# Kernel tuning notes

Measured on AMD Instinct MI355X. Metric: run time of the kernel, lower is better.

The kernel has to match this reference:

```python
import jax, jax.numpy as jnp
import numpy as np
import math

B, LQ, C = 4, 2048, 256
NH, NL, NP = 8, 4, 8
HD = C // NH
SHAPES = [(128, 128), (64, 64), (32, 32), (16, 16)]


def _grid_init_bias():
    thetas = np.arange(NH, dtype=np.float32) * (2.0 * math.pi / NH)
    g = np.stack([np.cos(thetas), np.sin(thetas)], -1)
    g = g / np.abs(g).max(-1, keepdims=True)
    g = np.tile(g[:, None, None, :], (1, NL, NP, 1))
    g = g * ((np.arange(NP, dtype=np.float32) + 1.0) / NP)[None, None, :, None]
    return jnp.asarray(g.reshape(-1), jnp.float32)


def setup_inputs() -> dict:
    key = jax.random.key(0)
    ks = jax.random.split(key, 12)
    Lv = sum(h * w for h, w in SHAPES)
    query = jax.random.normal(ks[0], (B, LQ, C), jnp.float32)
    reference_points = jax.random.uniform(ks[1], (B, LQ, NL, 2), jnp.float32)
    value = jax.random.normal(ks[2], (B, Lv, C), jnp.float32)
    spatial_shapes = jnp.asarray(np.array(SHAPES, np.int32))
    starts = np.cumsum([0] + [h * w for h, w in SHAPES])[:-1]
    level_start_index = jnp.asarray(starts.astype(np.int32))
    OFF = NH * NL * NP * 2
    return {
        'query': query,
        'reference_points': reference_points,
        'value': value,
        'spatial_shapes': spatial_shapes,
        'level_start_index': level_start_index,
        'W_off': jax.random.normal(ks[3], (C, OFF), jnp.float32) * 0.01,
        'b_off': _grid_init_bias(),
        'W_attn': jax.random.normal(ks[4], (C, NH * NL * NP), jnp.float32) * 0.01,
        'b_attn': jnp.zeros((NH * NL * NP,), jnp.float32),
        'Wa1': jax.random.normal(ks[5], (C, C // 2), jnp.float32) * 0.02,
        'ba1': jnp.zeros((C // 2,), jnp.float32),
        'Wa2': jax.random.normal(ks[6], (C // 2, OFF), jnp.float32) * 0.02,
        'ba2': jnp.zeros((OFF,), jnp.float32),
        'Wv': jax.random.normal(ks[7], (C, C), jnp.float32) * (1.0 / math.sqrt(C)),
        'bv': jnp.zeros((C,), jnp.float32),
        'Wo': jax.random.normal(ks[8], (C, C), jnp.float32) * (1.0 / math.sqrt(C)),
        'bo': jnp.zeros((C,), jnp.float32),
    }


def _bilinear(vflat, gx, gy, H, W):
    # vflat: [B, nh, H*W, hd]; gx, gy: [B, Lq, nh, P] in grid coords [-1, 1]
    # Matches F.grid_sample(mode='bilinear', padding_mode='zeros', align_corners=False)
    Bq, Lq, nh, P = gx.shape
    hd = vflat.shape[-1]
    x = ((gx + 1.0) * W - 1.0) * 0.5
    y = ((gy + 1.0) * H - 1.0) * 0.5
    x0f = jnp.floor(x); y0f = jnp.floor(y)
    lx = x - x0f; ly = y - y0f
    x0 = x0f.astype(jnp.int32); y0 = y0f.astype(jnp.int32)
    out = jnp.zeros((Bq, Lq, nh, P, hd), vflat.dtype)
    corners = ((0, 0, (1 - lx) * (1 - ly)), (1, 0, lx * (1 - ly)),
               (0, 1, (1 - lx) * ly), (1, 1, lx * ly))
    for dx, dy, w in corners:
        xi = x0 + dx; yi = y0 + dy
        valid = (xi >= 0) & (xi < W) & (yi >= 0) & (yi < H)
        idx = jnp.clip(yi, 0, H - 1) * W + jnp.clip(xi, 0, W - 1)
        idx_t = idx.transpose(0, 2, 1, 3).reshape(Bq, nh, Lq * P)
        g = jnp.take_along_axis(vflat, idx_t[..., None], axis=2)  # [B, nh, Lq*P, hd]
        g = g.reshape(Bq, nh, Lq, P, hd).transpose(0, 2, 1, 3, 4)
        out = out + g * (w * valid.astype(vflat.dtype))[..., None]
    return out


def reference(query, reference_points, value, spatial_shapes, level_start_index,
              W_off, b_off, W_attn, b_attn, Wa1, ba1, Wa2, ba2, Wv, bv, Wo, bo):
    shapes = np.asarray(spatial_shapes)
    starts = np.asarray(level_start_index)
    Bq, Lq, _ = query.shape

    v = (value @ Wv + bv).reshape(Bq, -1, NH, HD)            # [B, Lv, nh, hd]
    off = (query @ W_off + b_off).reshape(Bq, Lq, NH, NL, NP, 2)
    hid = jax.nn.relu(query @ Wa1 + ba1)
    off = off + 0.1 * (hid @ Wa2 + ba2).reshape(Bq, Lq, NH, NL, NP, 2)
    aw = jax.nn.softmax((query @ W_attn + b_attn).reshape(Bq, Lq, NH, NL * NP), -1)
    aw = aw.reshape(Bq, Lq, NH, NL, NP)

    # offset normalizer is (W, H) per level
    norm = jnp.stack([spatial_shapes[:, 1], spatial_shapes[:, 0]], -1).astype(query.dtype)
    loc = reference_points[:, :, None, :, None, :] + off / norm[None, None, None, :, None, :]
    grid = loc * 2.0 - 1.0                                    # [B, Lq, nh, NL, NP, 2]

    acc = jnp.zeros((Bq, Lq, NH, HD), query.dtype)
    for lvl in range(NL):
        H, W = int(shapes[lvl, 0]), int(shapes[lvl, 1])
        s = int(starts[lvl]); e = s + H * W
        vl = v[:, s:e].transpose(0, 2, 1, 3)                  # [B, nh, H*W, hd]
        gx = grid[:, :, :, lvl, :, 0]
        gy = grid[:, :, :, lvl, :, 1]
        samp = _bilinear(vl, gx, gy, H, W)                    # [B, Lq, nh, P, hd]
        acc = acc + jnp.einsum('blhpd,blhp->blhd', samp, aw[:, :, :, lvl, :])
    out = acc.reshape(Bq, Lq, NH * HD)
    return out @ Wo + bo
```

## Files before the change

kernel.cpp:

```cpp
#include <hip/hip_runtime.h>
#include <math.h>

#define B_SZ 4
#define LQ_SZ 2048
#define C_SZ 256
#define NH_SZ 8
#define NL_SZ 4
#define NP_SZ 8
#define HD_SZ 32
#define LV_SZ 21760
#define NQ_SZ (B_SZ * LQ_SZ)
#define MV_SZ (B_SZ * LV_SZ)

typedef __attribute__((ext_vector_type(8))) short bf16x8;
typedef __attribute__((ext_vector_type(8))) unsigned short ushort8;
typedef __attribute__((ext_vector_type(4))) float f32x4;

__device__ __forceinline__ float bf2f(unsigned short u) {
  union { float f; unsigned v; } x;
  x.v = ((unsigned)u) << 16;
  return x.f;
}
__device__ __forceinline__ unsigned short f2bf(float f) {
  union { float f; unsigned v; } x;
  x.f = f;
  unsigned r = x.v + 0x7fffu + ((x.v >> 16) & 1u);
  return (unsigned short)(r >> 16);
}

__device__ __forceinline__ bf16x8 cvt8(f32x4 a, f32x4 b) {
  union { unsigned u[4]; bf16x8 v; } r;
  asm("v_cvt_pk_bf16_f32 %0, %1, %2" : "=v"(r.u[0]) : "v"(a[0]), "v"(a[1]));
  asm("v_cvt_pk_bf16_f32 %0, %1, %2" : "=v"(r.u[1]) : "v"(a[2]), "v"(a[3]));
  asm("v_cvt_pk_bf16_f32 %0, %1, %2" : "=v"(r.u[2]) : "v"(b[0]), "v"(b[1]));
  asm("v_cvt_pk_bf16_f32 %0, %1, %2" : "=v"(r.u[3]) : "v"(b[2]), "v"(b[3]));
  return r.v;
}

__device__ __forceinline__ int swz(int x) {
  return ((x & 1) << 2) | ((x >> 1) & 3);
}

__global__ void prep_weights(
    const float* __restrict__ Wv, const float* __restrict__ Wo,
    const float* __restrict__ W_off, const float* __restrict__ W_attn,
    const float* __restrict__ Wa1, const float* __restrict__ Wa2,
    const float* __restrict__ b_off, const float* __restrict__ b_attn,
    const float* __restrict__ ba1,
    unsigned short* __restrict__ wtv, unsigned short* __restrict__ wto,
    unsigned short* __restrict__ wcat, unsigned short* __restrict__ wa2t,
    float* __restrict__ bcat) {
  const int bid = blockIdx.x, t = threadIdx.x;
  if (bid < 256) {
    wtv[bid * 256 + t] = f2bf(Wv[t * 256 + bid]);
  } else if (bid < 512) {
    const int n = bid - 256;
    wto[n * 256 + t] = f2bf(Wo[t * 256 + n]);
  } else if (bid < 1536) {
    const int n = bid - 512;
    float v;
    if (n < 512) v = W_off[t * 512 + n];
    else if (n < 768) v = W_attn[t * 256 + (n - 512)];
    else if (n < 896) v = Wa1[t * 128 + (n - 768)];
    else v = 0.f;
    wcat[n * 256 + t] = f2bf(v);
  } else if (bid < 1792) {
    const int idx = (bid - 1536) * 256 + t;
    const int n = idx >> 7, k = idx & 127;
    wa2t[n * 128 + k] = f2bf(Wa2[k * 512 + n]);
  } else {
    const int idx = (bid - 1792) * 256 + t;
    float v;
    if (idx < 512) v = b_off[idx];
    else if (idx < 768) v = b_attn[idx - 512];
    else if (idx < 896) v = ba1[idx - 768];
    else v = 0.f;
    bcat[idx] = v;
  }
}

template <int MODE, int A_BF16, int K_DIM>
__global__ __launch_bounds__(512, 2) void gemm_wave(
    const void* __restrict__ Ain, const unsigned short* __restrict__ Wt,
    const float* __restrict__ bias, void* __restrict__ Cout,
    unsigned short* __restrict__ aux, int n_total) {
  constexpr int KSTEPS = K_DIM / 32;
  constexpr int CHUNKS = K_DIM / 8;
  __shared__ unsigned short Bs[128 * K_DIM];
  const int tid = threadIdx.x;
  const int lane = tid & 63;
  const int w = tid >> 6;
  const int rowc = lane & 15, rowg = lane >> 4;
  const int bn0 = blockIdx.x * 128;
  const long bm = (long)blockIdx.y * 128;

  {
    const int row = tid >> 2, qq = tid & 3;
    const unsigned short* src = Wt + (long)(bn0 + row) * K_DIM;
    char* dstrow = (char*)Bs + row * (K_DIM * 2);
    const int sz = swz(row);
#pragma unroll
    for (int i = 0; i < CHUNKS / 4; ++i) {
      const int cl = i * 4 + qq;
      ushort8 u = *(const ushort8*)(src + cl * 8);
      *(ushort8*)(dstrow + (cl ^ sz) * 16) = u;
    }
  }

  bf16x8 afrag[KSTEPS];
  if constexpr (A_BF16) {
    const unsigned short* ap =
        (const unsigned short*)Ain + (bm + w * 16 + rowc) * (long)K_DIM +
        rowg * 8;
#pragma unroll
    for (int ks = 0; ks < KSTEPS; ++ks)
      afrag[ks] = *(const bf16x8*)(ap + ks * 32);
  } else {
    const float* ap =
        (const float*)Ain + (bm + w * 16 + rowc) * (long)K_DIM + rowg * 8;
#pragma unroll
    for (int ks = 0; ks < KSTEPS; ++ks) {
      f32x4 x0 = *(const f32x4*)(ap + ks * 32);
      f32x4 x1 = *(const f32x4*)(ap + ks * 32 + 4);
      afrag[ks] = cvt8(x0, x1);
    }
  }

  f32x4 acc[8];
#pragma unroll
  for (int n = 0; n < 8; ++n) acc[n] = (f32x4){0.f, 0.f, 0.f, 0.f};

  __syncthreads();

#pragma unroll
  for (int ks = 0; ks < KSTEPS; ++ks) {
#pragma unroll
    for (int n = 0; n < 8; ++n) {
      const int col = n * 16 + rowc;
      const int cs = (ks * 4 + rowg) ^ swz(col);
      bf16x8 bf =
          *(const bf16x8*)((const char*)Bs + col * (K_DIM * 2) + cs * 16);
      acc[n] = __builtin_amdgcn_mfma_f32_16x16x32_bf16(bf, afrag[ks], acc[n],
                                                       0, 0, 0);
    }
  }

  const long row = bm + w * 16 + rowc;
#pragma unroll
  for (int n = 0; n < 8; ++n) {
    const int col = bn0 + n * 16 + rowg * 4;
    const float4 bb = *(const float4*)(bias + col);
    const float v0 = acc[n][0] + bb.x;
    const float v1 = acc[n][1] + bb.y;
    const float v2 = acc[n][2] + bb.z;
    const float v3 = acc[n][3] + bb.w;
    if constexpr (MODE == 0) {
      float4 s = {v0, v1, v2, v3};
      *(float4*)((float*)Cout + row * n_total + col) = s;
    } else if constexpr (MODE == 1) {
      union { unsigned u[2]; uint2 d; } pk;
      asm("v_cvt_pk_bf16_f32 %0, %1, %2" : "=v"(pk.u[0]) : "v"(v0), "v"(v1));
      asm("v_cvt_pk_bf16_f32 %0, %1, %2" : "=v"(pk.u[1]) : "v"(v2), "v"(v3));
      *(uint2*)((unsigned short*)Cout + row * n_total + col) = pk.d;
    } else {
      if (bn0 < 768) {
        float4 s = {v0, v1, v2, v3};
        *(float4*)((float*)Cout + row * n_total + col) = s;
      } else {
        union { unsigned u[2]; uint2 d; } pk;
        const float r0 = fmaxf(v0, 0.f), r1 = fmaxf(v1, 0.f);
        const float r2 = fmaxf(v2, 0.f), r3 = fmaxf(v3, 0.f);
        asm("v_cvt_pk_bf16_f32 %0, %1, %2" : "=v"(pk.u[0]) : "v"(r0), "v"(r1));
        asm("v_cvt_pk_bf16_f32 %0, %1, %2" : "=v"(pk.u[1]) : "v"(r2), "v"(r3));
        *(uint2*)(aux + row * 128 + (col - 768)) = pk.d;
      }
    }
  }
}

__global__ __launch_bounds__(256) void sample_kernel(
    const unsigned short* __restrict__ v, const float* __restrict__ proj,
    const float* __restrict__ off2, const float* __restrict__ refpts,
    float* __restrict__ acc_out) {
  __shared__ int4 sidx[16 * 33];
  __shared__ float4 sw[16 * 33];
  const int tid = threadIdx.x;
  const long q0 = (long)blockIdx.x * 2;
  const int b = (int)(q0 >> 11);
  constexpr int starts[4] = {0, 16384, 20480, 21504};

#pragma unroll
  for (int ss = 0; ss < 2; ++ss) {
    const int s = tid + ss * 256;
    const int qq = s >> 8, j = s & 255;
    const long qi = q0 + qq;
    const int l = (j >> 3) & 3;
    const int HW = 128 >> l;
    const float fHW = (float)HW;
    const int slot = (qq * 8 + (j >> 5)) * 33 + (j & 31);

    const float logit = proj[qi * 1024 + 512 + j];
    float mx = logit;
#pragma unroll
    for (int mask = 16; mask > 0; mask >>= 1)
      mx = fmaxf(mx, __shfl_xor(mx, mask));
    const float e = __expf(logit - mx);
    float sum = e;
#pragma unroll
    for (int mask = 16; mask > 0; mask >>= 1) sum += __shfl_xor(sum, mask);
    const float wgt = e / sum;

    const float2 po = *(const float2*)(proj + qi * 1024 + 2 * j);
    const float2 o2 = *(const float2*)(off2 + qi * 512 + 2 * j);
    const float2 rp = *(const float2*)(refpts + qi * 8 + l * 2);
    const float rnorm = 1.f / fHW;
    const float gx = (rp.x + (po.x + 0.1f * o2.x) * rnorm) * 2.f - 1.f;
    const float gy = (rp.y + (po.y + 0.1f * o2.y) * rnorm) * 2.f - 1.f;

    const float x = ((gx + 1.f) * fHW - 1.f) * 0.5f;
    const float y = ((gy + 1.f) * fHW - 1.f) * 0.5f;
    const float x0f = floorf(x), y0f = floorf(y);
    const float lx = x - x0f, ly = y - y0f;
    const int ix0 = (int)x0f, iy0 = (int)y0f;
    const int ix1 = ix0 + 1, iy1 = iy0 + 1;
    const float vx0 = (ix0 >= 0 && ix0 < HW) ? 1.f : 0.f;
    const float vx1 = (ix1 >= 0 && ix1 < HW) ? 1.f : 0.f;
    const float vy0 = (iy0 >= 0 && iy0 < HW) ? 1.f : 0.f;
    const float vy1 = (iy1 >= 0 && iy1 < HW) ? 1.f : 0.f;
    const int cx0 = min(max(ix0, 0), HW - 1);
    const int cx1 = min(max(ix1, 0), HW - 1);
    const int cy0 = min(max(iy0, 0), HW - 1);
    const int cy1 = min(max(iy1, 0), HW - 1);
    const int base = starts[l];
    int4 o;
    o.x = (base + cy0 * HW + cx0) * 512;
    o.y = (base + cy0 * HW + cx1) * 512;
    o.z = (base + cy1 * HW + cx0) * 512;
    o.w = (base + cy1 * HW + cx1) * 512;
    sidx[slot] = o;
    float4 wv;
    wv.x = (1.f - lx) * (1.f - ly) * vx0 * vy0 * wgt;
    wv.y = lx * (1.f - ly) * vx1 * vy0 * wgt;
    wv.z = (1.f - lx) * ly * vx0 * vy1 * wgt;
    wv.w = lx * ly * vx1 * vy1 * wgt;
    sw[slot] = wv;
  }
  __syncthreads();

  const int qq = tid >> 7, h = (tid >> 4) & 7, dp = tid & 15;
  const char* vb =
      (const char*)v + ((long)b * LV_SZ * 256 + h * 32 + dp * 2) * 2;
  const int sbase = (qq * 8 + h) * 33;
  float acc0 = 0.f, acc1 = 0.f;
#pragma unroll 8
  for (int j = 0; j < 32; ++j) {
    const int4 o = sidx[sbase + j];
    const float4 w = sw[sbase + j];
    const ushort2 u0 = *(const ushort2*)(vb + o.x);
    const ushort2 u1 = *(const ushort2*)(vb + o.y);
    const ushort2 u2 = *(const ushort2*)(vb + o.z);
    const ushort2 u3 = *(const ushort2*)(vb + o.w);
    acc0 = fmaf(bf2f(u0.x), w.x, acc0);
    acc1 = fmaf(bf2f(u0.y), w.x, acc1);
    acc0 = fmaf(bf2f(u1.x), w.y, acc0);
    acc1 = fmaf(bf2f(u1.y), w.y, acc1);
    acc0 = fmaf(bf2f(u2.x), w.z, acc0);
    acc1 = fmaf(bf2f(u2.y), w.z, acc1);
    acc0 = fmaf(bf2f(u3.x), w.w, acc0);
    acc1 = fmaf(bf2f(u3.y), w.w, acc1);
  }
  float2 res = {acc0, acc1};
  *(float2*)(acc_out + (q0 + qq) * 256 + h * 32 + dp * 2) = res;
}

extern "C" void kernel_launch(void* const* d_in, const int* in_sizes, int n_in,
                              void* d_out, int out_size, void* d_ws,
                              size_t ws_size, hipStream_t stream) {
  const float* query  = (const float*)d_in[0];
  const float* refpts = (const float*)d_in[1];
  const float* value  = (const float*)d_in[2];
  const float* W_off  = (const float*)d_in[5];
  const float* b_off  = (const float*)d_in[6];
  const float* W_attn = (const float*)d_in[7];
  const float* b_attn = (const float*)d_in[8];
  const float* Wa1    = (const float*)d_in[9];
  const float* ba1    = (const float*)d_in[10];
  const float* Wa2    = (const float*)d_in[11];
  const float* ba2    = (const float*)d_in[12];
  const float* Wv     = (const float*)d_in[13];
  const float* bv     = (const float*)d_in[14];
  const float* Wo     = (const float*)d_in[15];
  const float* bo     = (const float*)d_in[16];
  float* out = (float*)d_out;

  char* ws = (char*)d_ws;
  unsigned short* v_ws = (unsigned short*)ws;
  float* proj_ws = (float*)(ws + 44564480);
  float* off2_ws = (float*)(ws + 78118912);
  unsigned short* wcat_ws = (unsigned short*)(ws + 78118912);
  unsigned short* hidb_ws = (unsigned short*)(ws + 94896128);
  float* acc_ws  = (float*)(ws + 96993280);
  unsigned short* wtv_ws  = (unsigned short*)(ws + 122159104);
  unsigned short* wto_ws  = (unsigned short*)(ws + 122290176);
  unsigned short* wa2t_ws = (unsigned short*)(ws + 122421248);
  float* bcat_ws = (float*)(ws + 122552320);

  prep_weights<<<1796, 256, 0, stream>>>(Wv, Wo, W_off, W_attn, Wa1, Wa2,
                                         b_off, b_attn, ba1, wtv_ws, wto_ws,
                                         wcat_ws, wa2t_ws, bcat_ws);
  gemm_wave<1, 0, 256><<<dim3(2, MV_SZ / 128), 512, 0, stream>>>(
      value, wtv_ws, bv, v_ws, nullptr, 256);
  gemm_wave<2, 0, 256><<<dim3(7, NQ_SZ / 128), 512, 0, stream>>>(
      query, wcat_ws, bcat_ws, proj_ws, hidb_ws, 1024);
  gemm_wave<0, 1, 128><<<dim3(4, NQ_SZ / 128), 512, 0, stream>>>(
      hidb_ws, wa2t_ws, ba2, off2_ws, nullptr, 512);
  sample_kernel<<<NQ_SZ / 2, 256, 0, stream>>>(v_ws, proj_ws, off2_ws, refpts,
                                               acc_ws);
  gemm_wave<0, 0, 256><<<dim3(2, NQ_SZ / 128), 512, 0, stream>>>(
      acc_ws, wto_ws, bo, out, nullptr, 256);
}
```

Before: 122.8 us.

## Shrink GEMM blocks to 64 rows and stage weights in 128-wide K phases

The wave-level MFMA GEMM now uses 256-thread blocks covering 64 rows instead of 512 threads covering 128 rows. Weight tiles are staged through a fixed 128x128 LDS buffer over K phases with barriers in between, instead of loading the full K extent at once. This cuts LDS use per block so more blocks can be resident per CU and the grid gets finer. In exchange each weight tile is reloaded by twice as many blocks, and the phased staging adds extra synchronisation.

```diff
diff --git a/kernel.cpp b/kernel.cpp
--- a/kernel.cpp
+++ b/kernel.cpp
@@ -80,46 +80,32 @@
 }
 
 template <int MODE, int A_BF16, int K_DIM>
-__global__ __launch_bounds__(512, 2) void gemm_wave(
+__global__ __launch_bounds__(256, 5) void gemm_wave2(
     const void* __restrict__ Ain, const unsigned short* __restrict__ Wt,
     const float* __restrict__ bias, void* __restrict__ Cout,
     unsigned short* __restrict__ aux, int n_total) {
-  constexpr int KSTEPS = K_DIM / 32;
-  constexpr int CHUNKS = K_DIM / 8;
-  __shared__ unsigned short Bs[128 * K_DIM];
+  constexpr int KPHASES = K_DIM / 128;
+  __shared__ unsigned short Bs[128 * 128];
   const int tid = threadIdx.x;
   const int lane = tid & 63;
   const int w = tid >> 6;
   const int rowc = lane & 15, rowg = lane >> 4;
   const int bn0 = blockIdx.x * 128;
-  const long bm = (long)blockIdx.y * 128;
-
-  {
-    const int row = tid >> 2, qq = tid & 3;
-    const unsigned short* src = Wt + (long)(bn0 + row) * K_DIM;
-    char* dstrow = (char*)Bs + row * (K_DIM * 2);
-    const int sz = swz(row);
-#pragma unroll
-    for (int i = 0; i < CHUNKS / 4; ++i) {
-      const int cl = i * 4 + qq;
-      ushort8 u = *(const ushort8*)(src + cl * 8);
-      *(ushort8*)(dstrow + (cl ^ sz) * 16) = u;
-    }
-  }
-
-  bf16x8 afrag[KSTEPS];
+  const long bm = (long)blockIdx.y * 64;
+
+  bf16x8 afrag[K_DIM / 32];
   if constexpr (A_BF16) {
     const unsigned short* ap =
         (const unsigned short*)Ain + (bm + w * 16 + rowc) * (long)K_DIM +
         rowg * 8;
 #pragma unroll
-    for (int ks = 0; ks < KSTEPS; ++ks)
+    for (int ks = 0; ks < K_DIM / 32; ++ks)
       afrag[ks] = *(const bf16x8*)(ap + ks * 32);
   } else {
     const float* ap =
         (const float*)Ain + (bm + w * 16 + rowc) * (long)K_DIM + rowg * 8;
 #pragma unroll
-    for (int ks = 0; ks < KSTEPS; ++ks) {
+    for (int ks = 0; ks < K_DIM / 32; ++ks) {
       f32x4 x0 = *(const f32x4*)(ap + ks * 32);
       f32x4 x1 = *(const f32x4*)(ap + ks * 32 + 4);
       afrag[ks] = cvt8(x0, x1);
@@ -130,18 +116,33 @@
 #pragma unroll
   for (int n = 0; n < 8; ++n) acc[n] = (f32x4){0.f, 0.f, 0.f, 0.f};
 
-  __syncthreads();
-
-#pragma unroll
-  for (int ks = 0; ks < KSTEPS; ++ks) {
-#pragma unroll
-    for (int n = 0; n < 8; ++n) {
-      const int col = n * 16 + rowc;
-      const int cs = (ks * 4 + rowg) ^ swz(col);
-      bf16x8 bf =
-          *(const bf16x8*)((const char*)Bs + col * (K_DIM * 2) + cs * 16);
-      acc[n] = __builtin_amdgcn_mfma_f32_16x16x32_bf16(bf, afrag[ks], acc[n],
-                                                       0, 0, 0);
+  const int srow = tid >> 1;
+  const int sqq = tid & 1;
+  const unsigned short* srcB = Wt + (long)(bn0 + srow) * K_DIM;
+  char* dstrow = (char*)Bs + srow * 256;
+  const int sz = swz(srow);
+
+#pragma unroll
+  for (int p = 0; p < KPHASES; ++p) {
+    if (p) __syncthreads();
+#pragma unroll
+    for (int i = 0; i < 8; ++i) {
+      const int cl = p * 16 + i * 2 + sqq;
+      ushort8 u = *(const ushort8*)(srcB + cl * 8);
+      *(ushort8*)(dstrow + ((cl & 15) ^ sz) * 16) = u;
+    }
+    __syncthreads();
+#pragma unroll
+    for (int kl = 0; kl < 4; ++kl) {
+      const int ks = p * 4 + kl;
+#pragma unroll
+      for (int n = 0; n < 8; ++n) {
+        const int col = n * 16 + rowc;
+        const int cs = (kl * 4 + rowg) ^ swz(col);
+        bf16x8 bf = *(const bf16x8*)((const char*)Bs + col * 256 + cs * 16);
+        acc[n] = __builtin_amdgcn_mfma_f32_16x16x32_bf16(bf, afrag[ks],
+                                                         acc[n], 0, 0, 0);
+      }
     }
   }
 
@@ -308,14 +309,14 @@
   prep_weights<<<1796, 256, 0, stream>>>(Wv, Wo, W_off, W_attn, Wa1, Wa2,
                                          b_off, b_attn, ba1, wtv_ws, wto_ws,
                                          wcat_ws, wa2t_ws, bcat_ws);
-  gemm_wave<1, 0, 256><<<dim3(2, MV_SZ / 128), 512, 0, stream>>>(
+  gemm_wave2<1, 0, 256><<<dim3(2, MV_SZ / 64), 256, 0, stream>>>(
       value, wtv_ws, bv, v_ws, nullptr, 256);
-  gemm_wave<2, 0, 256><<<dim3(7, NQ_SZ / 128), 512, 0, stream>>>(
+  gemm_wave2<2, 0, 256><<<dim3(7, NQ_SZ / 64), 256, 0, stream>>>(
       query, wcat_ws, bcat_ws, proj_ws, hidb_ws, 1024);
-  gemm_wave<0, 1, 128><<<dim3(4, NQ_SZ / 128), 512, 0, stream>>>(
+  gemm_wave2<0, 1, 128><<<dim3(4, NQ_SZ / 64), 256, 0, stream>>>(
       hidb_ws, wa2t_ws, ba2, off2_ws, nullptr, 512);
   sample_kernel<<<NQ_SZ / 2, 256, 0, stream>>>(v_ws, proj_ws, off2_ws, refpts,
                                                acc_ws);
-  gemm_wave<0, 0, 256><<<dim3(2, NQ_SZ / 128), 512, 0, stream>>>(
+  gemm_wave2<0, 0, 256><<<dim3(2, NQ_SZ / 64), 256, 0, stream>>>(
       acc_ws, wto_ws, bo, out, nullptr, 256);
 }
```

Measured after the change: 149.5 us. 21.8% more time.
